# Optimization experiments

Hardware: AMD Instinct MI355X
Metric: run time of the kernel (lower is better)

Reference implementation:

```python
import jax, jax.numpy as jnp
import numpy as np

N_NODES = 15000
N_EDGES = 40000
N_GRAPHS = 750
D = 64
NODE_DIM = 32
EDGE_DIM = 16
NUM_CONV = 3
S2S_STEPS = 3


def setup_inputs() -> dict:
    key = jax.random.key(0)
    ks = jax.random.split(key, 24)
    s = 0.05
    inp = {
        'x': jax.random.normal(ks[0], (N_NODES, NODE_DIM), jnp.float32),
        'edge_attr': jax.random.uniform(ks[1], (N_EDGES, EDGE_DIM), jnp.float32),
        'edge_index': jax.random.randint(ks[2], (2, N_EDGES), 0, N_NODES),
        'batch': jnp.sort(jax.random.randint(ks[3], (N_NODES,), 0, N_GRAPHS)),
        # input projection
        'in_W': jax.random.normal(ks[4], (NODE_DIM, D)) * s,
        'in_b': jnp.zeros((D,)),
        # edge MLP -> per-edge DxD weights
        'e1_W': jax.random.normal(ks[5], (EDGE_DIM, D)) * s,
        'e1_b': jnp.zeros((D,)),
        'e2_W': jax.random.normal(ks[6], (D, D * D)) * s,
        'e2_b': jnp.zeros((D * D,)),
        'conv_b': jnp.zeros((D,)),
        # GRU (gate order r,z,n like torch)
        'gru_Wih': jax.random.normal(ks[7], (3 * D, D)) * s,
        'gru_Whh': jax.random.normal(ks[8], (3 * D, D)) * s,
        'gru_bih': jnp.zeros((3 * D,)),
        'gru_bhh': jnp.zeros((3 * D,)),
        # Set2Set LSTM (gate order i,f,g,o like torch), input 2D -> hidden D
        'lstm_Wih': jax.random.normal(ks[9], (4 * D, 2 * D)) * s,
        'lstm_Whh': jax.random.normal(ks[10], (4 * D, D)) * s,
        'lstm_bih': jnp.zeros((4 * D,)),
        'lstm_bhh': jnp.zeros((4 * D,)),
        # output MLP
        'out1_W': jax.random.normal(ks[11], (2 * D, 2 * D)) * s,
        'out1_b': jnp.zeros((2 * D,)),
        'out2_W': jax.random.normal(ks[12], (2 * D, 1)) * s,
        'out2_b': jnp.zeros((1,)),
    }
    return inp


def _gru_cell(m, h, Wih, Whh, bih, bhh):
    gi = m @ Wih.T + bih
    gh = h @ Whh.T + bhh
    ir, iz, inn = jnp.split(gi, 3, axis=-1)
    hr, hz, hn = jnp.split(gh, 3, axis=-1)
    r = jax.nn.sigmoid(ir + hr)
    z = jax.nn.sigmoid(iz + hz)
    n = jnp.tanh(inn + r * hn)
    return (1.0 - z) * n + z * h


def _lstm_cell(q, h, c, Wih, Whh, bih, bhh):
    g = q @ Wih.T + bih + h @ Whh.T + bhh
    i, f, gg, o = jnp.split(g, 4, axis=-1)
    c = jax.nn.sigmoid(f) * c + jax.nn.sigmoid(i) * jnp.tanh(gg)
    h = jax.nn.sigmoid(o) * jnp.tanh(c)
    return h, c


def reference(x, edge_attr, edge_index, batch,
              in_W, in_b, e1_W, e1_b, e2_W, e2_b, conv_b,
              gru_Wih, gru_Whh, gru_bih, gru_bhh,
              lstm_Wih, lstm_Whh, lstm_bih, lstm_bhh,
              out1_W, out1_b, out2_W, out2_b):
    src, dst = edge_index[0], edge_index[1]
    out = jax.nn.relu(x @ in_W + in_b)           # [N, D]
    h = out
    # edge-conditioned weights (edge_attr is constant across conv iters)
    W_e = (jax.nn.relu(edge_attr @ e1_W + e1_b) @ e2_W + e2_b).reshape(-1, D, D)  # [E, D, D]
    deg = jnp.maximum(jax.ops.segment_sum(jnp.ones((N_EDGES,), out.dtype), dst, N_NODES), 1.0)
    for _ in range(NUM_CONV):
        msg = jnp.einsum('ed,edf->ef', out[src], W_e)          # per-edge matmul
        agg = jax.ops.segment_sum(msg, dst, N_NODES) / deg[:, None]  # scatter-mean
        m = jax.nn.relu(agg + conv_b)
        h = _gru_cell(m, h, gru_Wih, gru_Whh, gru_bih, gru_bhh)
        out = h
    # Set2Set pooling
    q_star = jnp.zeros((N_GRAPHS, 2 * D), out.dtype)
    hl = jnp.zeros((N_GRAPHS, D), out.dtype)
    cl = jnp.zeros((N_GRAPHS, D), out.dtype)
    for _ in range(S2S_STEPS):
        hl, cl = _lstm_cell(q_star, hl, cl, lstm_Wih, lstm_Whh, lstm_bih, lstm_bhh)
        q = hl
        e = jnp.sum(out * q[batch], axis=-1)                    # [N]
        e = e - jax.ops.segment_max(e, batch, N_GRAPHS)[batch]
        ee = jnp.exp(e)
        a = ee / jax.ops.segment_sum(ee, batch, N_GRAPHS)[batch]
        r = jax.ops.segment_sum(a[:, None] * out, batch, N_GRAPHS)  # [G, D]
        q_star = jnp.concatenate([q, r], axis=-1)
    z = jax.nn.relu(q_star @ out1_W + out1_b) @ out2_W + out2_b
    return z
```

## Files before the change

### kernel.cpp

```cpp
#include <hip/hip_runtime.h>
#include <math.h>

#define N_NODES 15000
#define N_EDGES 40000
#define N_GRAPHS 750
#define N_TILES 938
#define N_TILES_PAD 944

typedef __attribute__((ext_vector_type(8))) short bf16x8;
typedef __attribute__((ext_vector_type(4))) float f32x4;

__device__ __forceinline__ float sigmoidf_(float x) { return 1.f / (1.f + expf(-x)); }

__device__ __forceinline__ unsigned short f2bf(float v) {
    unsigned u = __float_as_uint(v);
    unsigned r = (u + 0x7FFFu + ((u >> 16) & 1u)) >> 16;
    return (unsigned short)r;
}
__device__ __forceinline__ float bf2f(unsigned short b) {
    return __uint_as_float(((unsigned)b) << 16);
}

__global__ void tscan_kernel(const int* __restrict__ tcnt, int* __restrict__ tptr,
                             int* __restrict__ cursor) {
    __shared__ int buf[1024];
    int t = threadIdx.x;
    int v = (t < N_TILES) ? tcnt[t] : 0;
    buf[t] = v;
    __syncthreads();
    for (int ofs = 1; ofs < 1024; ofs <<= 1) {
        int a = (t >= ofs) ? buf[t - ofs] : 0;
        __syncthreads();
        buf[t] += a;
        __syncthreads();
    }
    int excl = buf[t] - v;
    if (t <= N_TILES_PAD) tptr[t] = excl;
    if (t < N_TILES) cursor[t] = excl;
}

__global__ void fill_kernel(const int* __restrict__ src, int* __restrict__ cursor,
                            int* __restrict__ edge_list) {
    int e = blockIdx.x * 256 + threadIdx.x;
    if (e >= N_EDGES) return;
    int slot = atomicAdd(&cursor[src[e] >> 4], 1);
    edge_list[slot] = e;
}

__global__ __launch_bounds__(256)
void prep_kernel(const float* __restrict__ x, const float* __restrict__ in_W,
                 const float* __restrict__ in_b, float* __restrict__ node_h,
                 const float* __restrict__ e2b, float* __restrict__ Tb_g,
                 const float* __restrict__ ea, const float* __restrict__ e1_W,
                 const float* __restrict__ e1_b, float* __restrict__ h1,
                 const float* __restrict__ e2W,
                 unsigned short* __restrict__ Bhi, unsigned short* __restrict__ Blo,
                 const float* __restrict__ lWih, const float* __restrict__ lWhh,
                 const float* __restrict__ gWih, const float* __restrict__ gWhh,
                 float* __restrict__ lWihT, float* __restrict__ lWhhT,
                 unsigned short* __restrict__ gWihP, unsigned short* __restrict__ gWhhP,
                 unsigned short* __restrict__ e2bP,
                 const int* __restrict__ batch, int* __restrict__ gptr,
                 const int* __restrict__ src, const int* __restrict__ dst,
                 int* __restrict__ tcnt, float* __restrict__ deg) {
    int b = blockIdx.x;
    int tid = threadIdx.x;
    if (b < 3750) {
        __shared__ float xs[4][32];
        __shared__ float hrow[4][64];
        int n0 = b * 4;
        if (tid < 128) xs[tid >> 5][tid & 31] = x[n0 * 32 + tid];
        __syncthreads();
        int nn = tid >> 6, f = tid & 63;
        float s = in_b[f];
        #pragma unroll
        for (int i = 0; i < 32; ++i) s += xs[nn][i] * in_W[i * 64 + f];
        s = fmaxf(s, 0.f);
        node_h[(size_t)(n0 + nn) * 64 + f] = s;
        hrow[nn][f] = s;
        __syncthreads();
        float t2 = 0.f;
        #pragma unroll 8
        for (int d = 0; d < 64; ++d) t2 += hrow[nn][d] * e2b[d * 64 + f];
        Tb_g[(size_t)(n0 + nn) * 64 + f] = t2;
    } else if (b < 13750) {
        __shared__ float eas[4][16];
        int e0 = (b - 3750) * 4;
        if (tid < 64) eas[tid >> 4][tid & 15] = ea[e0 * 16 + tid];
        __syncthreads();
        int nn = tid >> 6, f = tid & 63;
        float s = e1_b[f];
        #pragma unroll
        for (int i = 0; i < 16; ++i) s += eas[nn][i] * e1_W[i * 64 + f];
        h1[(size_t)(e0 + nn) * 64 + f] = fmaxf(s, 0.f);
    } else if (b < 14774) {
        int idx = (b - 13750) * 256 + tid;
        int j = idx & 7, lane = (idx >> 3) & 63, kt = (idx >> 9) & 1;
        int ct = (idx >> 10) & 31, ft = idx >> 15;
        int d = kt * 32 + ((lane >> 4) << 3) + j;
        int c = ct * 16 + (lane & 15);
        int kk = c >> 3, fi = c & 7;
        float v = e2W[(size_t)kk * 4096 + d * 64 + ft * 8 + fi];
        unsigned short hi = f2bf(v);
        Bhi[idx] = hi;
        Blo[idx] = f2bf(v - bf2f(hi));
    } else if (b < 14966) {
        int idx = (b - 14774) * 256 + tid;
        if (idx < 32768) {
            int i = idx >> 8, r = idx & 255;
            lWihT[i * 256 + r] = lWih[r * 128 + i];
        } else if (idx < 49152) {
            int x2 = idx - 32768; int i = x2 >> 8, r = x2 & 255;
            lWhhT[i * 256 + r] = lWhh[r * 64 + i];
        }
    } else if (b < 15078) {
        int idx = (b - 14966) * 256 + tid;
        if (idx < 12288) {
            int j = idx & 7, lane = (idx >> 3) & 63, kt = (idx >> 9) & 1, ct = idx >> 10;
            int k = kt * 32 + ((lane >> 4) << 3) + j;
            int n = ct * 16 + (lane & 15);
            float v = gWih[n * 64 + k];
            unsigned short hi = f2bf(v);
            gWihP[idx] = hi;
            gWihP[12288 + idx] = f2bf(v - bf2f(hi));
        } else if (idx < 24576) {
            int i2 = idx - 12288;
            int j = i2 & 7, lane = (i2 >> 3) & 63, kt = (i2 >> 9) & 1, ct = i2 >> 10;
            int k = kt * 32 + ((lane >> 4) << 3) + j;
            int n = ct * 16 + (lane & 15);
            float v = gWhh[n * 64 + k];
            unsigned short hi = f2bf(v);
            gWhhP[i2] = hi;
            gWhhP[12288 + i2] = f2bf(v - bf2f(hi));
        } else {
            int i2 = idx - 24576;
            int j = i2 & 7, lane = (i2 >> 3) & 63, kt = (i2 >> 9) & 1, ct = i2 >> 10;
            int k = kt * 32 + ((lane >> 4) << 3) + j;
            int n = ct * 16 + (lane & 15);
            float v = e2b[k * 64 + n];
            unsigned short hi = f2bf(v);
            e2bP[i2] = hi;
            e2bP[4096 + i2] = f2bf(v - bf2f(hi));
        }
    } else if (b < 15137) {
        int n = (b - 15078) * 256 + tid;
        if (n < N_NODES) {
            int bb = batch[n];
            int pb = (n == 0) ? -1 : batch[n - 1];
            for (int g = pb + 1; g <= bb; ++g) gptr[g] = n;
            if (n == N_NODES - 1)
                for (int g = bb + 1; g <= N_GRAPHS; ++g) gptr[g] = N_NODES;
        }
    } else {
        int e = (b - 15137) * 256 + tid;
        if (e < N_EDGES) {
            atomicAdd(&tcnt[src[e] >> 4], 1);
            atomicAdd(&deg[dst[e]], 1.f);
        }
    }
}

__global__ __launch_bounds__(256, 4)
void conv_kernel(const float* __restrict__ node_h, const float* __restrict__ h1,
                 const unsigned short* __restrict__ Bhi, const unsigned short* __restrict__ Blo,
                 const float* __restrict__ Tb_g,
                 const int* __restrict__ tptr, const int* __restrict__ edge_list,
                 const int* __restrict__ src, const int* __restrict__ dst,
                 float* __restrict__ agg) {
    __shared__ float A_s[16][68];
    __shared__ float Tb_s[16][8];
    __shared__ float T_lds[16 * 548];
    int bid = blockIdx.x;
    int nt = bid % N_TILES_PAD, ft = bid / N_TILES_PAD;
    int n0 = nt * 16;
    int tid = threadIdx.x;

    {
        int nn = tid >> 4, d4 = (tid & 15) * 4;
        int n = n0 + nn;
        float4 v = make_float4(0.f, 0.f, 0.f, 0.f);
        if (n < N_NODES) v = *(const float4*)(node_h + (size_t)n * 64 + d4);
        *(float4*)(&A_s[nn][d4]) = v;
    }
    if (tid < 128) {
        int nn = tid >> 3, fi = tid & 7;
        int n = n0 + nn;
        Tb_s[nn][fi] = (n < N_NODES) ? Tb_g[(size_t)n * 64 + ft * 8 + fi] : 0.f;
    }
    __syncthreads();

    int lane = tid & 63, wave = tid >> 6;
    int quad = lane >> 4, m = lane & 15;

    bf16x8 ahi[2], alo[2];
    #pragma unroll
    for (int kt = 0; kt < 2; ++kt) {
        const float* ap = &A_s[m][kt * 32 + quad * 8];
        float4 x0 = *(const float4*)ap;
        float4 x1 = *(const float4*)(ap + 4);
        float av[8] = {x0.x, x0.y, x0.z, x0.w, x1.x, x1.y, x1.z, x1.w};
        #pragma unroll
        for (int j = 0; j < 8; ++j) {
            unsigned short hi = f2bf(av[j]);
            ahi[kt][j] = (short)hi;
            alo[kt][j] = (short)f2bf(av[j] - bf2f(hi));
        }
    }

    size_t base0 = ((size_t)((ft * 32 + wave * 8) * 2) * 64 + lane) * 8;
    const unsigned short* ph = Bhi + base0;
    const unsigned short* pl = Blo + base0;
    bf16x8 bh0 = *(const bf16x8*)(ph);
    bf16x8 bh1 = *(const bf16x8*)(ph + 512);
    bf16x8 bl0 = *(const bf16x8*)(pl);
    bf16x8 bl1 = *(const bf16x8*)(pl + 512);

    #pragma unroll 1
    for (int ci = 0; ci < 8; ++ci) {
        bf16x8 ch0 = bh0, ch1 = bh1, cl0 = bl0, cl1 = bl1;
        if (ci < 7) {
            const unsigned short* nh = ph + (ci + 1) * 1024;
            const unsigned short* nl = pl + (ci + 1) * 1024;
            bh0 = *(const bf16x8*)(nh);
            bh1 = *(const bf16x8*)(nh + 512);
            bl0 = *(const bf16x8*)(nl);
            bl1 = *(const bf16x8*)(nl + 512);
        }
        f32x4 accA = {0.f, 0.f, 0.f, 0.f};
        f32x4 accB = {0.f, 0.f, 0.f, 0.f};
        accA = __builtin_amdgcn_mfma_f32_16x16x32_bf16(ahi[0], ch0, accA, 0, 0, 0);
        accB = __builtin_amdgcn_mfma_f32_16x16x32_bf16(ahi[1], ch1, accB, 0, 0, 0);
        accA = __builtin_amdgcn_mfma_f32_16x16x32_bf16(alo[0], ch0, accA, 0, 0, 0);
        accB = __builtin_amdgcn_mfma_f32_16x16x32_bf16(alo[1], ch1, accB, 0, 0, 0);
        accA = __builtin_amdgcn_mfma_f32_16x16x32_bf16(ahi[0], cl0, accA, 0, 0, 0);
        accB = __builtin_amdgcn_mfma_f32_16x16x32_bf16(ahi[1], cl1, accB, 0, 0, 0);
        int c = (wave * 8 + ci) * 16 + m;
        int kk = c >> 3, fi = c & 7;
        #pragma unroll
        for (int r = 0; r < 4; ++r)
            T_lds[(quad * 4 + r) * 548 + fi * 68 + kk] = accA[r] + accB[r];
    }
    __syncthreads();

    int fi = tid & 7, slot = tid >> 3;
    int te0 = tptr[nt], te1 = tptr[nt + 1];
    for (int c = te0 + slot; c < te1; c += 32) {
        int e = edge_list[c];
        int nn = src[e] - n0;
        const float* h1e = h1 + (size_t)e * 64;
        const float* Tr = &T_lds[nn * 548 + fi * 68];
        float p0 = Tb_s[nn][fi], p1 = 0.f, p2 = 0.f, p3 = 0.f;
        #pragma unroll
        for (int k4 = 0; k4 < 64; k4 += 16) {
            float4 ha = *(const float4*)(h1e + k4);
            float4 ta = *(const float4*)(Tr + k4);
            float4 hb = *(const float4*)(h1e + k4 + 4);
            float4 tb = *(const float4*)(Tr + k4 + 4);
            float4 hc = *(const float4*)(h1e + k4 + 8);
            float4 tc = *(const float4*)(Tr + k4 + 8);
            float4 hd = *(const float4*)(h1e + k4 + 12);
            float4 td = *(const float4*)(Tr + k4 + 12);
            p0 += ha.x * ta.x + ha.y * ta.y + ha.z * ta.z + ha.w * ta.w;
            p1 += hb.x * tb.x + hb.y * tb.y + hb.z * tb.z + hb.w * tb.w;
            p2 += hc.x * tc.x + hc.y * tc.y + hc.z * tc.z + hc.w * tc.w;
            p3 += hd.x * td.x + hd.y * td.y + hd.z * td.z + hd.w * td.w;
        }
        float s = (p0 + p1) + (p2 + p3);
        atomicAdd(&agg[(size_t)dst[e] * 64 + ft * 8 + fi], s);
    }
}

__global__ __launch_bounds__(256, 4)
void gru_kernel(float* __restrict__ node_h, float* __restrict__ agg,
                const float* __restrict__ deg, const float* __restrict__ conv_b,
                const unsigned short* __restrict__ WihP, const unsigned short* __restrict__ WhhP,
                const float* __restrict__ bih, const float* __restrict__ bhh,
                const unsigned short* __restrict__ e2bP,
                float* __restrict__ Tb_g, int want_tb) {
    __shared__ unsigned short m_bf[2][32][72];
    __shared__ unsigned short h_bf[2][32][72];
    __shared__ unsigned short hn_bf[2][32][72];
    __shared__ float h_s[32][68];
    int n0 = blockIdx.x * 32;
    int tid = threadIdx.x;
    int lane = tid & 63, w = tid >> 6;
    int quad = lane >> 4, m16 = lane & 15;

    for (int i = tid; i < 2048; i += 256) {
        int c = i >> 6, f = i & 63;
        int n = n0 + c;
        float mv = 0.f, hv = 0.f;
        if (n < N_NODES) {
            float dg = fmaxf(deg[n], 1.f);
            mv = fmaxf(agg[(size_t)n * 64 + f] / dg + conv_b[f], 0.f);
            agg[(size_t)n * 64 + f] = 0.f;
            hv = node_h[(size_t)n * 64 + f];
        }
        unsigned short mh = f2bf(mv);
        m_bf[0][c][f] = mh; m_bf[1][c][f] = f2bf(mv - bf2f(mh));
        unsigned short hh = f2bf(hv);
        h_bf[0][c][f] = hh; h_bf[1][c][f] = f2bf(hv - bf2f(hh));
        h_s[c][f] = hv;
    }

    bf16x8 Bi[3][2][2], Bh[3][2][2];
    #pragma unroll
    for (int g = 0; g < 3; ++g)
        #pragma unroll
        for (int kt = 0; kt < 2; ++kt) {
            size_t base = ((size_t)((g * 4 + w) * 2 + kt) * 64 + lane) * 8;
            Bi[g][kt][0] = *(const bf16x8*)(WihP + base);
            Bi[g][kt][1] = *(const bf16x8*)(WihP + 12288 + base);
            Bh[g][kt][0] = *(const bf16x8*)(WhhP + base);
            Bh[g][kt][1] = *(const bf16x8*)(WhhP + 12288 + base);
        }
    int f = w * 16 + m16;
    float br_i = bih[f],       br_h = bhh[f];
    float bz_i = bih[64 + f],  bz_h = bhh[64 + f];
    float bn_i = bih[128 + f], bn_h = bhh[128 + f];
    __syncthreads();

    #pragma unroll 1
    for (int mt = 0; mt < 2; ++mt) {
        bf16x8 Am[2][2], Ah[2][2];
        #pragma unroll
        for (int kt = 0; kt < 2; ++kt) {
            Am[kt][0] = *(const bf16x8*)(&m_bf[0][mt * 16 + m16][kt * 32 + quad * 8]);
            Am[kt][1] = *(const bf16x8*)(&m_bf[1][mt * 16 + m16][kt * 32 + quad * 8]);
            Ah[kt][0] = *(const bf16x8*)(&h_bf[0][mt * 16 + m16][kt * 32 + quad * 8]);
            Ah[kt][1] = *(const bf16x8*)(&h_bf[1][mt * 16 + m16][kt * 32 + quad * 8]);
        }
        f32x4 ai[3], ah[3];
        #pragma unroll
        for (int g = 0; g < 3; ++g) { ai[g] = (f32x4){0.f,0.f,0.f,0.f}; ah[g] = (f32x4){0.f,0.f,0.f,0.f}; }
        #pragma unroll
        for (int g = 0; g < 3; ++g)
            #pragma unroll
            for (int kt = 0; kt < 2; ++kt) {
                ai[g] = __builtin_amdgcn_mfma_f32_16x16x32_bf16(Am[kt][0], Bi[g][kt][0], ai[g], 0, 0, 0);
                ai[g] = __builtin_amdgcn_mfma_f32_16x16x32_bf16(Am[kt][0], Bi[g][kt][1], ai[g], 0, 0, 0);
                ai[g] = __builtin_amdgcn_mfma_f32_16x16x32_bf16(Am[kt][1], Bi[g][kt][0], ai[g], 0, 0, 0);
                ah[g] = __builtin_amdgcn_mfma_f32_16x16x32_bf16(Ah[kt][0], Bh[g][kt][0], ah[g], 0, 0, 0);
                ah[g] = __builtin_amdgcn_mfma_f32_16x16x32_bf16(Ah[kt][0], Bh[g][kt][1], ah[g], 0, 0, 0);
                ah[g] = __builtin_amdgcn_mfma_f32_16x16x32_bf16(Ah[kt][1], Bh[g][kt][0], ah[g], 0, 0, 0);
            }
        #pragma unroll
        for (int r = 0; r < 4; ++r) {
            int node = mt * 16 + quad * 4 + r;
            float rr = sigmoidf_(ai[0][r] + br_i + ah[0][r] + br_h);
            float zz = sigmoidf_(ai[1][r] + bz_i + ah[1][r] + bz_h);
            float n2 = tanhf(ai[2][r] + bn_i + rr * (ah[2][r] + bn_h));
            float hnew = (1.f - zz) * n2 + zz * h_s[node][f];
            int n = n0 + node;
            if (n < N_NODES) node_h[(size_t)n * 64 + f] = hnew;
            unsigned short hh = f2bf(hnew);
            hn_bf[0][node][f] = hh;
            hn_bf[1][node][f] = f2bf(hnew - bf2f(hh));
        }
    }
    if (want_tb) {
        __syncthreads();
        bf16x8 Eb[2][2];
        #pragma unroll
        for (int kt = 0; kt < 2; ++kt) {
            size_t base = ((size_t)((w * 2 + kt) * 64) + lane) * 8;
            Eb[kt][0] = *(const bf16x8*)(e2bP + base);
            Eb[kt][1] = *(const bf16x8*)(e2bP + 4096 + base);
        }
        #pragma unroll 1
        for (int mt = 0; mt < 2; ++mt) {
            bf16x8 A2[2][2];
            #pragma unroll
            for (int kt = 0; kt < 2; ++kt) {
                A2[kt][0] = *(const bf16x8*)(&hn_bf[0][mt * 16 + m16][kt * 32 + quad * 8]);
                A2[kt][1] = *(const bf16x8*)(&hn_bf[1][mt * 16 + m16][kt * 32 + quad * 8]);
            }
            f32x4 acc = {0.f, 0.f, 0.f, 0.f};
            #pragma unroll
            for (int kt = 0; kt < 2; ++kt) {
                acc = __builtin_amdgcn_mfma_f32_16x16x32_bf16(A2[kt][0], Eb[kt][0], acc, 0, 0, 0);
                acc = __builtin_amdgcn_mfma_f32_16x16x32_bf16(A2[kt][0], Eb[kt][1], acc, 0, 0, 0);
                acc = __builtin_amdgcn_mfma_f32_16x16x32_bf16(A2[kt][1], Eb[kt][0], acc, 0, 0, 0);
            }
            #pragma unroll
            for (int r = 0; r < 4; ++r) {
                int n = n0 + mt * 16 + quad * 4 + r;
                if (n < N_NODES) Tb_g[(size_t)n * 64 + f] = acc[r];
            }
        }
    }
}

__global__ __launch_bounds__(128)
void s2s_kernel(const float* __restrict__ node_h, const int* __restrict__ gptr,
                const float* __restrict__ WihT, const float* __restrict__ WhhT,
                const float* __restrict__ bih, const float* __restrict__ bhh,
                const float* __restrict__ o1W, const float* __restrict__ o1b,
                const float* __restrict__ o2W, const float* __restrict__ o2b,
                float* __restrict__ z) {
    int g = blockIdx.x, tid = threadIdx.x;
    int f = tid & 63, half = tid >> 6;
    __shared__ float qs[128], hs[64], q[64], wts[128], gvs[4][64], racc_s[2][64];
    __shared__ float mred[2], sred[2], ored[2];
    if (half == 0) { qs[f] = 0.f; qs[64 + f] = 0.f; hs[f] = 0.f; }
    float c_t = 0.f;
    int nbeg = gptr[g], nend = gptr[g + 1];
    __syncthreads();
    for (int st = 0; st < 3; ++st) {
        #pragma unroll
        for (int gg = 0; gg < 2; ++gg) {
            int gate = half * 2 + gg;
            int row = gate * 64 + f;
            float s = bih[row] + bhh[row];
            #pragma unroll 8
            for (int i = 0; i < 128; ++i) s += qs[i] * WihT[i * 256 + row];
            #pragma unroll 8
            for (int i = 0; i < 64; ++i) s += hs[i] * WhhT[i * 256 + row];
            gvs[gate][f] = s;
        }
        __syncthreads();
        if (half == 0) {
            float c = sigmoidf_(gvs[1][f]) * c_t + sigmoidf_(gvs[0][f]) * tanhf(gvs[2][f]);
            float hn = sigmoidf_(gvs[3][f]) * tanhf(c);
            c_t = c;
            hs[f] = hn; q[f] = hn;
        }
        __syncthreads();
        float rm = -INFINITY, rs = 0.f, raccl = 0.f;
        for (int base = nbeg; base < nend; base += 128) {
            int n = base + tid;
            float e = -INFINITY;
            if (n < nend) {
                float s = 0.f;
                #pragma unroll 8
                for (int ff = 0; ff < 64; ++ff) s += node_h[(size_t)n * 64 + ff] * q[ff];
                e = s;
            }
            float cm = e;
            #pragma unroll
            for (int o = 32; o > 0; o >>= 1) cm = fmaxf(cm, __shfl_down(cm, o));
            if ((tid & 63) == 0) mred[half] = cm;
            __syncthreads();
            float bm = fmaxf(mred[0], mred[1]);
            float nm = fmaxf(rm, bm);
            float scale = (rm == -INFINITY) ? 0.f : expf(rm - nm);
            float wv = (n < nend) ? expf(e - nm) : 0.f;
            wts[tid] = wv;
            float cs = wv;
            #pragma unroll
            for (int o = 32; o > 0; o >>= 1) cs += __shfl_down(cs, o);
            if ((tid & 63) == 0) sred[half] = cs;
            __syncthreads();
            float bs = sred[0] + sred[1];
            float na = raccl * scale;
            int cnt2 = min(128, nend - base);
            int l0 = half * 64, l1 = min(l0 + 64, cnt2);
            for (int l = l0; l < l1; ++l) na += wts[l] * node_h[(size_t)(base + l) * 64 + f];
            raccl = na;
            rs = rs * scale + bs;
            rm = nm;
            __syncthreads();
        }
        racc_s[half][f] = raccl;
        __syncthreads();
        if (half == 0) {
            float r = (nend > nbeg) ? (racc_s[0][f] + racc_s[1][f]) / rs : 0.f;
            qs[f] = q[f];
            qs[64 + f] = r;
        }
        __syncthreads();
    }
    float sA = o1b[tid];
    #pragma unroll 8
    for (int i = 0; i < 128; ++i) sA += qs[i] * o1W[i * 128 + tid];
    float red = fmaxf(sA, 0.f) * o2W[tid];
    #pragma unroll
    for (int o = 32; o > 0; o >>= 1) red += __shfl_down(red, o);
    if ((tid & 63) == 0) ored[half] = red;
    __syncthreads();
    if (tid == 0) z[g] = ored[0] + ored[1] + o2b[0];
}

extern "C" void kernel_launch(void* const* d_in, const int* in_sizes, int n_in,
                              void* d_out, int out_size, void* d_ws, size_t ws_size,
                              hipStream_t stream) {
    const float* x         = (const float*)d_in[0];
    const float* edge_attr = (const float*)d_in[1];
    const int*   ei        = (const int*)d_in[2];
    const int*   batch     = (const int*)d_in[3];
    const float* in_W      = (const float*)d_in[4];
    const float* in_b      = (const float*)d_in[5];
    const float* e1_W      = (const float*)d_in[6];
    const float* e1_b      = (const float*)d_in[7];
    const float* e2_W      = (const float*)d_in[8];
    const float* e2_b      = (const float*)d_in[9];
    const float* conv_b    = (const float*)d_in[10];
    const float* gWih      = (const float*)d_in[11];
    const float* gWhh      = (const float*)d_in[12];
    const float* gbih      = (const float*)d_in[13];
    const float* gbhh      = (const float*)d_in[14];
    const float* lWih      = (const float*)d_in[15];
    const float* lWhh      = (const float*)d_in[16];
    const float* lbih      = (const float*)d_in[17];
    const float* lbhh      = (const float*)d_in[18];
    const float* o1W       = (const float*)d_in[19];
    const float* o1b       = (const float*)d_in[20];
    const float* o2W       = (const float*)d_in[21];
    const float* o2b       = (const float*)d_in[22];
    const int* src = ei;
    const int* dst = ei + N_EDGES;
    float* z = (float*)d_out;

    char* ws = (char*)d_ws;
    size_t off = 0;
    auto alloc = [&](size_t bytes) {
        void* p = ws + off;
        off = (off + bytes + 255) & ~(size_t)255;
        return p;
    };
    float* node_h   = (float*)alloc((size_t)N_NODES * 64 * 4);
    float* agg      = (float*)alloc((size_t)N_NODES * 64 * 4);
    float* h1       = (float*)alloc((size_t)N_EDGES * 64 * 4);
    unsigned short* Bhi = (unsigned short*)alloc((size_t)262144 * 2);
    unsigned short* Blo = (unsigned short*)alloc((size_t)262144 * 2);
    float* Tb_g     = (float*)alloc((size_t)N_NODES * 64 * 4);
    float* lWihT    = (float*)alloc(128 * 256 * 4);
    float* lWhhT    = (float*)alloc(64 * 256 * 4);
    unsigned short* gWihP = (unsigned short*)alloc(24576 * 2);
    unsigned short* gWhhP = (unsigned short*)alloc(24576 * 2);
    unsigned short* e2bP  = (unsigned short*)alloc(8192 * 2);
    float* deg      = (float*)alloc(N_NODES * 4);
    int*   tcnt     = (int*)alloc((N_TILES + 2) * 4);
    int*   tcursor  = (int*)alloc((N_TILES + 2) * 4);
    int*   tptr     = (int*)alloc((N_TILES_PAD + 2) * 4);
    int*   edge_list= (int*)alloc(N_EDGES * 4);
    int*   gptr     = (int*)alloc((N_GRAPHS + 1) * 4);

    size_t degpad = ((size_t)N_NODES * 4 + 255) & ~(size_t)255;
    hipMemsetAsync(deg, 0, degpad + (N_TILES + 2) * 4, stream);
    hipMemsetAsync(agg, 0, (size_t)N_NODES * 64 * 4, stream);

    prep_kernel<<<15294, 256, 0, stream>>>(x, in_W, in_b, node_h, e2_b, Tb_g,
                                           edge_attr, e1_W, e1_b, h1,
                                           e2_W, Bhi, Blo,
                                           lWih, lWhh, gWih, gWhh,
                                           lWihT, lWhhT, gWihP, gWhhP, e2bP,
                                           batch, gptr, src, dst, tcnt, deg);
    tscan_kernel<<<1, 1024, 0, stream>>>(tcnt, tptr, tcursor);
    fill_kernel<<<(N_EDGES + 255) / 256, 256, 0, stream>>>(src, tcursor, edge_list);

    for (int it = 0; it < 3; ++it) {
        conv_kernel<<<N_TILES_PAD * 8, 256, 0, stream>>>(node_h, h1, Bhi, Blo, Tb_g,
                                                         tptr, edge_list, src, dst, agg);
        gru_kernel<<<469, 256, 0, stream>>>(node_h, agg, deg, conv_b,
                                            gWihP, gWhhP, gbih, gbhh,
                                            e2bP, Tb_g, (it < 2) ? 1 : 0);
    }
    s2s_kernel<<<N_GRAPHS, 128, 0, stream>>>(node_h, gptr, lWihT, lWhhT, lbih, lbhh,
                                             o1W, o1b, o2W, o2b, z);
}
```

Baseline: 444.1 us.

## Fold e2 bias projection into conv MFMA as extra column tile

Removes the separate Tb (h @ e2_b) computation from the prep and GRU kernels. It adds the bias matrix as a 33rd column tile of the packed B operand, so the conv kernel's MFMA produces it directly into T_lds (read at column 64). The per-edge loop is also unrolled to process two edges per thread iteration. This saves the Tb_g global writes and reads and the extra MFMAs in the GRU kernel. In exchange, wave 0 does a ninth tile, which makes the waves unbalanced.

```diff
diff --git a/kernel.cpp b/kernel.cpp
--- a/kernel.cpp
+++ b/kernel.cpp
@@ -50,7 +50,7 @@
 __global__ __launch_bounds__(256)
 void prep_kernel(const float* __restrict__ x, const float* __restrict__ in_W,
                  const float* __restrict__ in_b, float* __restrict__ node_h,
-                 const float* __restrict__ e2b, float* __restrict__ Tb_g,
+                 const float* __restrict__ e2b,
                  const float* __restrict__ ea, const float* __restrict__ e1_W,
                  const float* __restrict__ e1_b, float* __restrict__ h1,
                  const float* __restrict__ e2W,
@@ -59,7 +59,6 @@
                  const float* __restrict__ gWih, const float* __restrict__ gWhh,
                  float* __restrict__ lWihT, float* __restrict__ lWhhT,
                  unsigned short* __restrict__ gWihP, unsigned short* __restrict__ gWhhP,
-                 unsigned short* __restrict__ e2bP,
                  const int* __restrict__ batch, int* __restrict__ gptr,
                  const int* __restrict__ src, const int* __restrict__ dst,
                  int* __restrict__ tcnt, float* __restrict__ deg) {
@@ -67,7 +66,6 @@
     int tid = threadIdx.x;
     if (b < 3750) {
         __shared__ float xs[4][32];
-        __shared__ float hrow[4][64];
         int n0 = b * 4;
         if (tid < 128) xs[tid >> 5][tid & 31] = x[n0 * 32 + tid];
         __syncthreads();
@@ -75,14 +73,7 @@
         float s = in_b[f];
         #pragma unroll
         for (int i = 0; i < 32; ++i) s += xs[nn][i] * in_W[i * 64 + f];
-        s = fmaxf(s, 0.f);
-        node_h[(size_t)(n0 + nn) * 64 + f] = s;
-        hrow[nn][f] = s;
-        __syncthreads();
-        float t2 = 0.f;
-        #pragma unroll 8
-        for (int d = 0; d < 64; ++d) t2 += hrow[nn][d] * e2b[d * 64 + f];
-        Tb_g[(size_t)(n0 + nn) * 64 + f] = t2;
+        node_h[(size_t)(n0 + nn) * 64 + f] = fmaxf(s, 0.f);
     } else if (b < 13750) {
         __shared__ float eas[4][16];
         int e0 = (b - 3750) * 4;
@@ -93,19 +84,26 @@
         #pragma unroll
         for (int i = 0; i < 16; ++i) s += eas[nn][i] * e1_W[i * 64 + f];
         h1[(size_t)(e0 + nn) * 64 + f] = fmaxf(s, 0.f);
-    } else if (b < 14774) {
+    } else if (b < 14806) {
         int idx = (b - 13750) * 256 + tid;
         int j = idx & 7, lane = (idx >> 3) & 63, kt = (idx >> 9) & 1;
-        int ct = (idx >> 10) & 31, ft = idx >> 15;
+        int rem = idx >> 10;
+        int ct = rem % 33, ft = rem / 33;
         int d = kt * 32 + ((lane >> 4) << 3) + j;
-        int c = ct * 16 + (lane & 15);
-        int kk = c >> 3, fi = c & 7;
-        float v = e2W[(size_t)kk * 4096 + d * 64 + ft * 8 + fi];
+        int m = lane & 15;
+        float v;
+        if (ct < 32) {
+            int c = ct * 16 + m;
+            int kk = c >> 3, fi = c & 7;
+            v = e2W[(size_t)kk * 4096 + d * 64 + ft * 8 + fi];
+        } else {
+            v = (m < 8) ? e2b[d * 64 + ft * 8 + m] : 0.f;
+        }
         unsigned short hi = f2bf(v);
         Bhi[idx] = hi;
         Blo[idx] = f2bf(v - bf2f(hi));
-    } else if (b < 14966) {
-        int idx = (b - 14774) * 256 + tid;
+    } else if (b < 14998) {
+        int idx = (b - 14806) * 256 + tid;
         if (idx < 32768) {
             int i = idx >> 8, r = idx & 255;
             lWihT[i * 256 + r] = lWih[r * 128 + i];
@@ -113,8 +111,8 @@
             int x2 = idx - 32768; int i = x2 >> 8, r = x2 & 255;
             lWhhT[i * 256 + r] = lWhh[r * 64 + i];
         }
-    } else if (b < 15078) {
-        int idx = (b - 14966) * 256 + tid;
+    } else if (b < 15094) {
+        int idx = (b - 14998) * 256 + tid;
         if (idx < 12288) {
             int j = idx & 7, lane = (idx >> 3) & 63, kt = (idx >> 9) & 1, ct = idx >> 10;
             int k = kt * 32 + ((lane >> 4) << 3) + j;
@@ -123,7 +121,7 @@
             unsigned short hi = f2bf(v);
             gWihP[idx] = hi;
             gWihP[12288 + idx] = f2bf(v - bf2f(hi));
-        } else if (idx < 24576) {
+        } else {
             int i2 = idx - 12288;
             int j = i2 & 7, lane = (i2 >> 3) & 63, kt = (i2 >> 9) & 1, ct = i2 >> 10;
             int k = kt * 32 + ((lane >> 4) << 3) + j;
@@ -132,18 +130,9 @@
             unsigned short hi = f2bf(v);
             gWhhP[i2] = hi;
             gWhhP[12288 + i2] = f2bf(v - bf2f(hi));
-        } else {
-            int i2 = idx - 24576;
-            int j = i2 & 7, lane = (i2 >> 3) & 63, kt = (i2 >> 9) & 1, ct = i2 >> 10;
-            int k = kt * 32 + ((lane >> 4) << 3) + j;
-            int n = ct * 16 + (lane & 15);
-            float v = e2b[k * 64 + n];
-            unsigned short hi = f2bf(v);
-            e2bP[i2] = hi;
-            e2bP[4096 + i2] = f2bf(v - bf2f(hi));
-        }
-    } else if (b < 15137) {
-        int n = (b - 15078) * 256 + tid;
+        }
+    } else if (b < 15153) {
+        int n = (b - 15094) * 256 + tid;
         if (n < N_NODES) {
             int bb = batch[n];
             int pb = (n == 0) ? -1 : batch[n - 1];
@@ -152,7 +141,7 @@
                 for (int g = bb + 1; g <= N_GRAPHS; ++g) gptr[g] = N_NODES;
         }
     } else {
-        int e = (b - 15137) * 256 + tid;
+        int e = (b - 15153) * 256 + tid;
         if (e < N_EDGES) {
             atomicAdd(&tcnt[src[e] >> 4], 1);
             atomicAdd(&deg[dst[e]], 1.f);
@@ -163,12 +152,10 @@
 __global__ __launch_bounds__(256, 4)
 void conv_kernel(const float* __restrict__ node_h, const float* __restrict__ h1,
                  const unsigned short* __restrict__ Bhi, const unsigned short* __restrict__ Blo,
-                 const float* __restrict__ Tb_g,
                  const int* __restrict__ tptr, const int* __restrict__ edge_list,
                  const int* __restrict__ src, const int* __restrict__ dst,
                  float* __restrict__ agg) {
     __shared__ float A_s[16][68];
-    __shared__ float Tb_s[16][8];
     __shared__ float T_lds[16 * 548];
     int bid = blockIdx.x;
     int nt = bid % N_TILES_PAD, ft = bid / N_TILES_PAD;
@@ -181,11 +168,6 @@
         float4 v = make_float4(0.f, 0.f, 0.f, 0.f);
         if (n < N_NODES) v = *(const float4*)(node_h + (size_t)n * 64 + d4);
         *(float4*)(&A_s[nn][d4]) = v;
-    }
-    if (tid < 128) {
-        int nn = tid >> 3, fi = tid & 7;
-        int n = n0 + nn;
-        Tb_s[nn][fi] = (n < N_NODES) ? Tb_g[(size_t)n * 64 + ft * 8 + fi] : 0.f;
     }
     __syncthreads();
 
@@ -207,7 +189,7 @@
         }
     }
 
-    size_t base0 = ((size_t)((ft * 32 + wave * 8) * 2) * 64 + lane) * 8;
+    size_t base0 = (size_t)(ft * 33 + wave) * 1024 + lane * 8;
     const unsigned short* ph = Bhi + base0;
     const unsigned short* pl = Blo + base0;
     bf16x8 bh0 = *(const bf16x8*)(ph);
@@ -215,12 +197,13 @@
     bf16x8 bl0 = *(const bf16x8*)(pl);
     bf16x8 bl1 = *(const bf16x8*)(pl + 512);
 
+    int nct = (wave == 0) ? 9 : 8;
     #pragma unroll 1
-    for (int ci = 0; ci < 8; ++ci) {
+    for (int ci = 0; ci < nct; ++ci) {
         bf16x8 ch0 = bh0, ch1 = bh1, cl0 = bl0, cl1 = bl1;
-        if (ci < 7) {
-            const unsigned short* nh = ph + (ci + 1) * 1024;
-            const unsigned short* nl = pl + (ci + 1) * 1024;
+        if (ci + 1 < nct) {
+            const unsigned short* nh = ph + (size_t)(ci + 1) * 4096;
+            const unsigned short* nl = pl + (size_t)(ci + 1) * 4096;
             bh0 = *(const bf16x8*)(nh);
             bh1 = *(const bf16x8*)(nh + 512);
             bl0 = *(const bf16x8*)(nl);
@@ -234,7 +217,8 @@
         accB = __builtin_amdgcn_mfma_f32_16x16x32_bf16(alo[1], ch1, accB, 0, 0, 0);
         accA = __builtin_amdgcn_mfma_f32_16x16x32_bf16(ahi[0], cl0, accA, 0, 0, 0);
         accB = __builtin_amdgcn_mfma_f32_16x16x32_bf16(ahi[1], cl1, accB, 0, 0, 0);
-        int c = (wave * 8 + ci) * 16 + m;
+        int ct = wave + ci * 4;
+        int c = ct * 16 + m;
         int kk = c >> 3, fi = c & 7;
         #pragma unroll
         for (int r = 0; r < 4; ++r)
@@ -244,29 +228,35 @@
 
     int fi = tid & 7, slot = tid >> 3;
     int te0 = tptr[nt], te1 = tptr[nt + 1];
-    for (int c = te0 + slot; c < te1; c += 32) {
-        int e = edge_list[c];
-        int nn = src[e] - n0;
-        const float* h1e = h1 + (size_t)e * 64;
-        const float* Tr = &T_lds[nn * 548 + fi * 68];
-        float p0 = Tb_s[nn][fi], p1 = 0.f, p2 = 0.f, p3 = 0.f;
-        #pragma unroll
-        for (int k4 = 0; k4 < 64; k4 += 16) {
-            float4 ha = *(const float4*)(h1e + k4);
-            float4 ta = *(const float4*)(Tr + k4);
-            float4 hb = *(const float4*)(h1e + k4 + 4);
-            float4 tb = *(const float4*)(Tr + k4 + 4);
-            float4 hc = *(const float4*)(h1e + k4 + 8);
-            float4 tc = *(const float4*)(Tr + k4 + 8);
-            float4 hd = *(const float4*)(h1e + k4 + 12);
-            float4 td = *(const float4*)(Tr + k4 + 12);
-            p0 += ha.x * ta.x + ha.y * ta.y + ha.z * ta.z + ha.w * ta.w;
-            p1 += hb.x * tb.x + hb.y * tb.y + hb.z * tb.z + hb.w * tb.w;
-            p2 += hc.x * tc.x + hc.y * tc.y + hc.z * tc.z + hc.w * tc.w;
-            p3 += hd.x * td.x + hd.y * td.y + hd.z * td.z + hd.w * td.w;
-        }
-        float s = (p0 + p1) + (p2 + p3);
-        atomicAdd(&agg[(size_t)dst[e] * 64 + ft * 8 + fi], s);
+    for (int c = te0 + slot; c < te1; c += 64) {
+        int c1 = c + 32;
+        bool h2 = (c1 < te1);
+        int e0 = edge_list[c];
+        int e1 = h2 ? edge_list[c1] : e0;
+        int nn0 = src[e0] - n0, nn1 = src[e1] - n0;
+        const float* h0p = h1 + (size_t)e0 * 64;
+        const float* h1p = h1 + (size_t)e1 * 64;
+        const float* T0 = &T_lds[nn0 * 548 + fi * 68];
+        const float* T1 = &T_lds[nn1 * 548 + fi * 68];
+        float p00 = T0[64], p01 = 0.f;
+        float p10 = T1[64], p11 = 0.f;
+        #pragma unroll
+        for (int k4 = 0; k4 < 64; k4 += 8) {
+            float4 ha = *(const float4*)(h0p + k4);
+            float4 ta = *(const float4*)(T0 + k4);
+            float4 hb = *(const float4*)(h0p + k4 + 4);
+            float4 tb = *(const float4*)(T0 + k4 + 4);
+            float4 hc = *(const float4*)(h1p + k4);
+            float4 tc = *(const float4*)(T1 + k4);
+            float4 hd = *(const float4*)(h1p + k4 + 4);
+            float4 td = *(const float4*)(T1 + k4 + 4);
+            p00 += ha.x * ta.x + ha.y * ta.y + ha.z * ta.z + ha.w * ta.w;
+            p01 += hb.x * tb.x + hb.y * tb.y + hb.z * tb.z + hb.w * tb.w;
+            p10 += hc.x * tc.x + hc.y * tc.y + hc.z * tc.z + hc.w * tc.w;
+            p11 += hd.x * td.x + hd.y * td.y + hd.z * td.z + hd.w * td.w;
+        }
+        atomicAdd(&agg[(size_t)dst[e0] * 64 + ft * 8 + fi], p00 + p01);
+        if (h2) atomicAdd(&agg[(size_t)dst[e1] * 64 + ft * 8 + fi], p10 + p11);
     }
 }
 
@@ -274,12 +264,9 @@
 void gru_kernel(float* __restrict__ node_h, float* __restrict__ agg,
                 const float* __restrict__ deg, const float* __restrict__ conv_b,
                 const unsigned short* __restrict__ WihP, const unsigned short* __restrict__ WhhP,
-                const float* __restrict__ bih, const float* __restrict__ bhh,
-                const unsigned short* __restrict__ e2bP,
-                float* __restrict__ Tb_g, int want_tb) {
+                const float* __restrict__ bih, const float* __restrict__ bhh) {
     __shared__ unsigned short m_bf[2][32][72];
     __shared__ unsigned short h_bf[2][32][72];
-    __shared__ unsigned short hn_bf[2][32][72];
     __shared__ float h_s[32][68];
     int n0 = blockIdx.x * 32;
     int tid = threadIdx.x;
@@ -353,40 +340,6 @@
             float hnew = (1.f - zz) * n2 + zz * h_s[node][f];
             int n = n0 + node;
             if (n < N_NODES) node_h[(size_t)n * 64 + f] = hnew;
-            unsigned short hh = f2bf(hnew);
-            hn_bf[0][node][f] = hh;
-            hn_bf[1][node][f] = f2bf(hnew - bf2f(hh));
-        }
-    }
-    if (want_tb) {
-        __syncthreads();
-        bf16x8 Eb[2][2];
-        #pragma unroll
-        for (int kt = 0; kt < 2; ++kt) {
-            size_t base = ((size_t)((w * 2 + kt) * 64) + lane) * 8;
-            Eb[kt][0] = *(const bf16x8*)(e2bP + base);
-            Eb[kt][1] = *(const bf16x8*)(e2bP + 4096 + base);
-        }
-        #pragma unroll 1
-        for (int mt = 0; mt < 2; ++mt) {
-            bf16x8 A2[2][2];
-            #pragma unroll
-            for (int kt = 0; kt < 2; ++kt) {
-                A2[kt][0] = *(const bf16x8*)(&hn_bf[0][mt * 16 + m16][kt * 32 + quad * 8]);
-                A2[kt][1] = *(const bf16x8*)(&hn_bf[1][mt * 16 + m16][kt * 32 + quad * 8]);
-            }
-            f32x4 acc = {0.f, 0.f, 0.f, 0.f};
-            #pragma unroll
-            for (int kt = 0; kt < 2; ++kt) {
-                acc = __builtin_amdgcn_mfma_f32_16x16x32_bf16(A2[kt][0], Eb[kt][0], acc, 0, 0, 0);
-                acc = __builtin_amdgcn_mfma_f32_16x16x32_bf16(A2[kt][0], Eb[kt][1], acc, 0, 0, 0);
-                acc = __builtin_amdgcn_mfma_f32_16x16x32_bf16(A2[kt][1], Eb[kt][0], acc, 0, 0, 0);
-            }
-            #pragma unroll
-            for (int r = 0; r < 4; ++r) {
-                int n = n0 + mt * 16 + quad * 4 + r;
-                if (n < N_NODES) Tb_g[(size_t)n * 64 + f] = acc[r];
-            }
         }
     }
 }
@@ -521,14 +474,12 @@
     float* node_h   = (float*)alloc((size_t)N_NODES * 64 * 4);
     float* agg      = (float*)alloc((size_t)N_NODES * 64 * 4);
     float* h1       = (float*)alloc((size_t)N_EDGES * 64 * 4);
-    unsigned short* Bhi = (unsigned short*)alloc((size_t)262144 * 2);
-    unsigned short* Blo = (unsigned short*)alloc((size_t)262144 * 2);
-    float* Tb_g     = (float*)alloc((size_t)N_NODES * 64 * 4);
+    unsigned short* Bhi = (unsigned short*)alloc((size_t)270336 * 2);
+    unsigned short* Blo = (unsigned short*)alloc((size_t)270336 * 2);
     float* lWihT    = (float*)alloc(128 * 256 * 4);
     float* lWhhT    = (float*)alloc(64 * 256 * 4);
     unsigned short* gWihP = (unsigned short*)alloc(24576 * 2);
     unsigned short* gWhhP = (unsigned short*)alloc(24576 * 2);
-    unsigned short* e2bP  = (unsigned short*)alloc(8192 * 2);
     float* deg      = (float*)alloc(N_NODES * 4);
     int*   tcnt     = (int*)alloc((N_TILES + 2) * 4);
     int*   tcursor  = (int*)alloc((N_TILES + 2) * 4);
@@ -540,21 +491,20 @@
     hipMemsetAsync(deg, 0, degpad + (N_TILES + 2) * 4, stream);
     hipMemsetAsync(agg, 0, (size_t)N_NODES * 64 * 4, stream);
 
-    prep_kernel<<<15294, 256, 0, stream>>>(x, in_W, in_b, node_h, e2_b, Tb_g,
+    prep_kernel<<<15310, 256, 0, stream>>>(x, in_W, in_b, node_h, e2_b,
                                            edge_attr, e1_W, e1_b, h1,
                                            e2_W, Bhi, Blo,
                                            lWih, lWhh, gWih, gWhh,
-                                           lWihT, lWhhT, gWihP, gWhhP, e2bP,
+                                           lWihT, lWhhT, gWihP, gWhhP,
                                            batch, gptr, src, dst, tcnt, deg);
     tscan_kernel<<<1, 1024, 0, stream>>>(tcnt, tptr, tcursor);
     fill_kernel<<<(N_EDGES + 255) / 256, 256, 0, stream>>>(src, tcursor, edge_list);
 
     for (int it = 0; it < 3; ++it) {
-        conv_kernel<<<N_TILES_PAD * 8, 256, 0, stream>>>(node_h, h1, Bhi, Blo, Tb_g,
+        conv_kernel<<<N_TILES_PAD * 8, 256, 0, stream>>>(node_h, h1, Bhi, Blo,
                                                          tptr, edge_list, src, dst, agg);
         gru_kernel<<<469, 256, 0, stream>>>(node_h, agg, deg, conv_b,
-                                            gWihP, gWhhP, gbih, gbhh,
-                                            e2bP, Tb_g, (it < 2) ? 1 : 0);
+                                            gWihP, gWhhP, gbih, gbhh);
     }
     s2s_kernel<<<N_GRAPHS, 128, 0, stream>>>(node_h, gptr, lWihT, lWhhT, lbih, lbhh,
                                              o1W, o1b, o2W, o2b, z);
```

Measured after the change: 432.3 us. 1.03x faster.
